# Kernel optimization log

Hardware: AMD Instinct MI355X
Metric: run time of the kernel (lower is better)

The kernel has to match this reference:

```python
import jax, jax.numpy as jnp
import numpy as np

C_IN = 256
A = 2086
H_BOARD, W_BOARD = 10, 9
S = H_BOARD * W_BOARD  # 90
E = 2                  # embed dim after 1x1 conv
NH = 2                 # num attention heads (head_dim = 1)
B = 4096
BN_EPS = 1e-5


def setup_inputs() -> dict:
    key = jax.random.key(0)
    ks = jax.random.split(key, 12)
    inp = {
        "x": jax.random.normal(ks[0], (B, C_IN, H_BOARD, W_BOARD), dtype=jnp.float32),
        # 1x1 conv, no bias: weight [out=2, in=256]
        "conv_w": jax.random.normal(ks[1], (E, C_IN), dtype=jnp.float32) * 0.05,
        # BatchNorm2d(2) params / running stats (inference-mode BN)
        "bn_gamma": jnp.ones((E,), dtype=jnp.float32),
        "bn_beta": jnp.zeros((E,), dtype=jnp.float32),
        "bn_mean": jax.random.normal(ks[2], (E,), dtype=jnp.float32) * 0.1,
        "bn_var": jax.random.uniform(ks[3], (E,), dtype=jnp.float32, minval=0.5, maxval=1.5),
        # MultiheadAttention packed in-proj: [3*E, E], bias [3*E]
        "in_proj_w": jax.random.normal(ks[4], (3 * E, E), dtype=jnp.float32) * 0.5,
        "in_proj_b": jax.random.normal(ks[5], (3 * E,), dtype=jnp.float32) * 0.05,
        "out_proj_w": jax.random.normal(ks[6], (E, E), dtype=jnp.float32) * 0.5,
        "out_proj_b": jax.random.normal(ks[7], (E,), dtype=jnp.float32) * 0.05,
        # Linear(2*90 -> 2086)
        "fc_w": jax.random.normal(ks[8], (A, E * S), dtype=jnp.float32) * 0.05,
        "fc_b": jax.random.normal(ks[9], (A,), dtype=jnp.float32) * 0.05,
    }
    return inp


def reference(x, conv_w, bn_gamma, bn_beta, bn_mean, bn_var,
              in_proj_w, in_proj_b, out_proj_w, out_proj_b, fc_w, fc_b):
    b = x.shape[0]
    # 1x1 conv (bias-free) == channel contraction: [b,256,h,w] -> [b,2,h,w]
    y = jnp.einsum('bchw,oc->bohw', x, conv_w)
    # BatchNorm2d (inference): (y - mean) / sqrt(var + eps) * gamma + beta
    scale = (bn_gamma * jax.lax.rsqrt(bn_var + BN_EPS))[None, :, None, None]
    shift = (bn_beta - bn_mean * bn_gamma * jax.lax.rsqrt(bn_var + BN_EPS))[None, :, None, None]
    y = y * scale + shift
    # [b,2,h,w] -> [b, S, 2]  (seq = board cells, feature = 2 channels)
    xf = y.reshape(b, E, S).transpose(0, 2, 1)
    # packed QKV projection
    qkv = xf @ in_proj_w.T + in_proj_b          # [b,S,3E]
    q, k, v = jnp.split(qkv, 3, axis=-1)        # each [b,S,E]
    hd = E // NH                                 # head_dim = 1
    def split_heads(t):
        return t.reshape(b, S, NH, hd).transpose(0, 2, 1, 3)  # [b,nh,S,hd]
    q, k, v = split_heads(q), split_heads(k), split_heads(v)
    scores = jnp.einsum('bhqd,bhkd->bhqk', q, k) / jnp.sqrt(jnp.float32(hd))
    attn = jax.nn.softmax(scores, axis=-1)      # [b,nh,S,S]
    o = jnp.einsum('bhqk,bhkd->bhqd', attn, v)  # [b,nh,S,hd]
    o = o.transpose(0, 2, 1, 3).reshape(b, S, E)
    o = o @ out_proj_w.T + out_proj_b           # [b,S,E]
    # [b,S,E] -> [b,E,S] -> [b, E*S], matching permute(0,2,1).view(b,-1)
    flat = o.transpose(0, 2, 1).reshape(b, E * S)
    logits = flat @ fc_w.T + fc_b               # [b, 2086]
    return logits
```

## Files before the change

kernel.cpp:

```cpp
#include <hip/hip_runtime.h>

#define C_IN    256
#define S_CELLS 90
#define A_OUT   2086
#define K_FC    180
#define K_PAD   192
#define N_PAD   2176
#define B_BATCH 4096

typedef __attribute__((ext_vector_type(8))) short short8;
typedef __attribute__((ext_vector_type(4))) float floatx4;

static __device__ __forceinline__ unsigned short f2bf(float f) {
    unsigned u = __float_as_uint(f);
    return (unsigned short)((u + 0x7FFFu + ((u >> 16) & 1u)) >> 16);
}

__global__ __launch_bounds__(384) void front_kernel(
    const float* __restrict__ x,
    const float* __restrict__ conv_w,
    const float* __restrict__ bn_gamma,
    const float* __restrict__ bn_beta,
    const float* __restrict__ bn_mean,
    const float* __restrict__ bn_var,
    const float* __restrict__ ipw,
    const float* __restrict__ ipb,
    const float* __restrict__ opw,
    const float* __restrict__ opb,
    unsigned short* __restrict__ Abf)
{
    __shared__ float4 kvpack[4][S_CELLS];

    const int sub = threadIdx.x / 96;
    const int s   = threadIdx.x % 96;
    const int b   = blockIdx.x * 4 + sub;

    float q0 = 0.f, q1 = 0.f;

    if (s < S_CELLS) {
        const float* xb = x + (size_t)b * (C_IN * S_CELLS) + s;
        float a0 = 0.f, a1 = 0.f;
        #pragma unroll 16
        for (int c = 0; c < C_IN; ++c) {
            float xv = xb[(size_t)c * S_CELLS];
            a0 = fmaf(conv_w[c], xv, a0);
            a1 = fmaf(conv_w[C_IN + c], xv, a1);
        }
        const float sc0 = bn_gamma[0] * rsqrtf(bn_var[0] + 1e-5f);
        const float sc1 = bn_gamma[1] * rsqrtf(bn_var[1] + 1e-5f);
        const float y0 = a0 * sc0 + (bn_beta[0] - bn_mean[0] * sc0);
        const float y1 = a1 * sc1 + (bn_beta[1] - bn_mean[1] * sc1);
        q0 = ipw[0] * y0 + ipw[1] * y1 + ipb[0];
        q1 = ipw[2] * y0 + ipw[3] * y1 + ipb[1];
        const float k0 = ipw[4] * y0 + ipw[5]  * y1 + ipb[2];
        const float k1 = ipw[6] * y0 + ipw[7]  * y1 + ipb[3];
        const float v0 = ipw[8] * y0 + ipw[9]  * y1 + ipb[4];
        const float v1 = ipw[10]* y0 + ipw[11] * y1 + ipb[5];
        kvpack[sub][s] = make_float4(k0, v0, k1, v1);
    }
    __syncthreads();
    if (s < S_CELLS) {
        float den0 = 0.f, num0 = 0.f, den1 = 0.f, num1 = 0.f;
        #pragma unroll 5
        for (int j = 0; j < S_CELLS; ++j) {
            const float4 kv = kvpack[sub][j];
            const float e0 = __expf(q0 * kv.x);
            const float e1 = __expf(q1 * kv.z);
            den0 += e0; num0 = fmaf(e0, kv.y, num0);
            den1 += e1; num1 = fmaf(e1, kv.w, num1);
        }
        const float o0 = num0 / den0;
        const float o1 = num1 / den1;
        const float r0 = opw[0] * o0 + opw[1] * o1 + opb[0];
        const float r1 = opw[2] * o0 + opw[3] * o1 + opb[1];
        Abf[(size_t)b * K_PAD + s]           = f2bf(r0);
        Abf[(size_t)b * K_PAD + S_CELLS + s] = f2bf(r1);
    } else {
        Abf[(size_t)b * K_PAD + 180 + (s - S_CELLS)] = 0;
        Abf[(size_t)b * K_PAD + 186 + (s - S_CELLS)] = 0;
    }
}

__global__ __launch_bounds__(192) void wconv_kernel(
    const float* __restrict__ W, unsigned short* __restrict__ Wbf)
{
    const int n = blockIdx.x;
    const int k = threadIdx.x;
    unsigned short v = 0;
    if (n < A_OUT && k < K_FC) v = f2bf(W[(size_t)n * K_FC + k]);
    Wbf[(size_t)n * K_PAD + k] = v;
}

#define BM 128
#define BN 128
#define BK 64
#define LDSROW 72

__global__ __launch_bounds__(256) void fc_mfma_kernel(
    const unsigned short* __restrict__ Abf,
    const unsigned short* __restrict__ Wbf,
    const float* __restrict__ bias,
    float* __restrict__ out)
{
    __shared__ __align__(16) unsigned short As[BM * LDSROW];
    __shared__ __align__(16) unsigned short Bs[BN * LDSROW];

    const int tid  = threadIdx.x;
    const int lane = tid & 63;
    const int wave = tid >> 6;
    const int wy   = wave >> 1;
    const int wx   = wave & 1;
    const int lrow = lane & 15;
    const int lk   = (lane >> 4) * 8;
    const int bm   = blockIdx.y * BM;
    const int bn   = blockIdx.x * BN;

    floatx4 acc[4][4] = {};

    for (int k0 = 0; k0 < K_PAD; k0 += BK) {
        for (int q = tid; q < BM * 8; q += 256) {
            const int m = q >> 3, c = q & 7;
            *(int4*)&As[m * LDSROW + c * 8] =
                *(const int4*)(Abf + (size_t)(bm + m) * K_PAD + k0 + c * 8);
            *(int4*)&Bs[m * LDSROW + c * 8] =
                *(const int4*)(Wbf + (size_t)(bn + m) * K_PAD + k0 + c * 8);
        }
        __syncthreads();

        #pragma unroll
        for (int ks = 0; ks < 2; ++ks) {
            short8 af[4], bf[4];
            #pragma unroll
            for (int t = 0; t < 4; ++t) {
                af[t] = *(const short8*)&As[(wy * 64 + t * 16 + lrow) * LDSROW + ks * 32 + lk];
                bf[t] = *(const short8*)&Bs[(wx * 64 + t * 16 + lrow) * LDSROW + ks * 32 + lk];
            }
            #pragma unroll
            for (int mt = 0; mt < 4; ++mt)
                #pragma unroll
                for (int nt = 0; nt < 4; ++nt)
                    acc[mt][nt] = __builtin_amdgcn_mfma_f32_16x16x32_bf16(
                        af[mt], bf[nt], acc[mt][nt], 0, 0, 0);
        }
        __syncthreads();
    }

    const int ccol = lane & 15;
    const int crow = (lane >> 4) * 4;
    #pragma unroll
    for (int mt = 0; mt < 4; ++mt) {
        #pragma unroll
        for (int nt = 0; nt < 4; ++nt) {
            const int n_out = bn + wx * 64 + nt * 16 + ccol;
            if (n_out >= A_OUT) continue;
            const int m_base = bm + wy * 64 + mt * 16 + crow;
            const float bv = bias[n_out];
            #pragma unroll
            for (int r = 0; r < 4; ++r)
                out[(size_t)(m_base + r) * A_OUT + n_out] = acc[mt][nt][r] + bv;
        }
    }
}

extern "C" void kernel_launch(void* const* d_in, const int* in_sizes, int n_in,
                              void* d_out, int out_size, void* d_ws, size_t ws_size,
                              hipStream_t stream) {
    const float* x        = (const float*)d_in[0];
    const float* conv_w   = (const float*)d_in[1];
    const float* bn_gamma = (const float*)d_in[2];
    const float* bn_beta  = (const float*)d_in[3];
    const float* bn_mean  = (const float*)d_in[4];
    const float* bn_var   = (const float*)d_in[5];
    const float* ipw      = (const float*)d_in[6];
    const float* ipb      = (const float*)d_in[7];
    const float* opw      = (const float*)d_in[8];
    const float* opb      = (const float*)d_in[9];
    const float* fc_w     = (const float*)d_in[10];
    const float* fc_b     = (const float*)d_in[11];
    float* out = (float*)d_out;

    unsigned short* Abf = (unsigned short*)d_ws;
    unsigned short* Wbf = (unsigned short*)((char*)d_ws + (size_t)B_BATCH * K_PAD * 2);

    front_kernel<<<dim3(B_BATCH / 4), 384, 0, stream>>>(
        x, conv_w, bn_gamma, bn_beta, bn_mean, bn_var,
        ipw, ipb, opw, opb, Abf);

    wconv_kernel<<<dim3(N_PAD), 192, 0, stream>>>(fc_w, Wbf);

    fc_mfma_kernel<<<dim3(N_PAD / BN, B_BATCH / BM), 256, 0, stream>>>(
        Abf, Wbf, fc_b, out);
}
```

Baseline: 545.2 us.

## Fuse FC weight bf16 conversion into GEMM loads and remap front kernel to one wave per board

Removes the separate weight-conversion kernel and instead converts fp32 fc_w to bf16 while staging it into LDS inside the MFMA GEMM, using zero padding for out-of-range rows and columns. This drops one launch and the round trip of the converted weights through memory. The cost is that every GEMM block redoes the conversion, 32 times per weight tile in total. The front kernel now gives each batch element one 64-lane wave that handles two cells per lane with float2 loads, and runs 8 boards per 512-thread block.

```diff
diff --git a/kernel.cpp b/kernel.cpp
--- a/kernel.cpp
+++ b/kernel.cpp
@@ -16,7 +16,7 @@
     return (unsigned short)((u + 0x7FFFu + ((u >> 16) & 1u)) >> 16);
 }
 
-__global__ __launch_bounds__(384) void front_kernel(
+__global__ __launch_bounds__(512) void front_kernel(
     const float* __restrict__ x,
     const float* __restrict__ conv_w,
     const float* __restrict__ bn_gamma,
@@ -29,66 +29,75 @@
     const float* __restrict__ opb,
     unsigned short* __restrict__ Abf)
 {
-    __shared__ float4 kvpack[4][S_CELLS];
-
-    const int sub = threadIdx.x / 96;
-    const int s   = threadIdx.x % 96;
-    const int b   = blockIdx.x * 4 + sub;
-
-    float q0 = 0.f, q1 = 0.f;
-
-    if (s < S_CELLS) {
-        const float* xb = x + (size_t)b * (C_IN * S_CELLS) + s;
-        float a0 = 0.f, a1 = 0.f;
-        #pragma unroll 16
+    __shared__ float4 kvs[8][S_CELLS];
+
+    const int wid  = threadIdx.x >> 6;
+    const int lane = threadIdx.x & 63;
+    const int b    = blockIdx.x * 8 + wid;
+
+    float qA0 = 0.f, qA1 = 0.f, qB0 = 0.f, qB1 = 0.f;
+    const int sA = 2 * lane;
+    const int sB = 2 * lane + 1;
+
+    if (lane < 45) {
+        const float2* xb2 = reinterpret_cast<const float2*>(
+                                x + (size_t)b * (C_IN * S_CELLS)) + lane;
+        float a00 = 0.f, a01 = 0.f, a10 = 0.f, a11 = 0.f;
+        #pragma unroll 8
         for (int c = 0; c < C_IN; ++c) {
-            float xv = xb[(size_t)c * S_CELLS];
-            a0 = fmaf(conv_w[c], xv, a0);
-            a1 = fmaf(conv_w[C_IN + c], xv, a1);
+            const float2 v = xb2[c * 45];
+            const float w0 = conv_w[c];
+            const float w1 = conv_w[C_IN + c];
+            a00 = fmaf(w0, v.x, a00); a01 = fmaf(w0, v.y, a01);
+            a10 = fmaf(w1, v.x, a10); a11 = fmaf(w1, v.y, a11);
         }
         const float sc0 = bn_gamma[0] * rsqrtf(bn_var[0] + 1e-5f);
         const float sc1 = bn_gamma[1] * rsqrtf(bn_var[1] + 1e-5f);
-        const float y0 = a0 * sc0 + (bn_beta[0] - bn_mean[0] * sc0);
-        const float y1 = a1 * sc1 + (bn_beta[1] - bn_mean[1] * sc1);
-        q0 = ipw[0] * y0 + ipw[1] * y1 + ipb[0];
-        q1 = ipw[2] * y0 + ipw[3] * y1 + ipb[1];
-        const float k0 = ipw[4] * y0 + ipw[5]  * y1 + ipb[2];
-        const float k1 = ipw[6] * y0 + ipw[7]  * y1 + ipb[3];
-        const float v0 = ipw[8] * y0 + ipw[9]  * y1 + ipb[4];
-        const float v1 = ipw[10]* y0 + ipw[11] * y1 + ipb[5];
-        kvpack[sub][s] = make_float4(k0, v0, k1, v1);
+        const float sh0 = bn_beta[0] - bn_mean[0] * sc0;
+        const float sh1 = bn_beta[1] - bn_mean[1] * sc1;
+        const float yA0 = a00 * sc0 + sh0, yA1 = a10 * sc1 + sh1;
+        const float yB0 = a01 * sc0 + sh0, yB1 = a11 * sc1 + sh1;
+
+        qA0 = ipw[0] * yA0 + ipw[1] * yA1 + ipb[0];
+        qA1 = ipw[2] * yA0 + ipw[3] * yA1 + ipb[1];
+        qB0 = ipw[0] * yB0 + ipw[1] * yB1 + ipb[0];
+        qB1 = ipw[2] * yB0 + ipw[3] * yB1 + ipb[1];
+
+        kvs[wid][sA] = make_float4(
+            ipw[4] * yA0 + ipw[5]  * yA1 + ipb[2],
+            ipw[8] * yA0 + ipw[9]  * yA1 + ipb[4],
+            ipw[6] * yA0 + ipw[7]  * yA1 + ipb[3],
+            ipw[10]* yA0 + ipw[11] * yA1 + ipb[5]);
+        kvs[wid][sB] = make_float4(
+            ipw[4] * yB0 + ipw[5]  * yB1 + ipb[2],
+            ipw[8] * yB0 + ipw[9]  * yB1 + ipb[4],
+            ipw[6] * yB0 + ipw[7]  * yB1 + ipb[3],
+            ipw[10]* yB0 + ipw[11] * yB1 + ipb[5]);
     }
     __syncthreads();
-    if (s < S_CELLS) {
-        float den0 = 0.f, num0 = 0.f, den1 = 0.f, num1 = 0.f;
+
+    if (lane < 45) {
+        float dA0 = 0.f, nA0 = 0.f, dA1 = 0.f, nA1 = 0.f;
+        float dB0 = 0.f, nB0 = 0.f, dB1 = 0.f, nB1 = 0.f;
         #pragma unroll 5
         for (int j = 0; j < S_CELLS; ++j) {
-            const float4 kv = kvpack[sub][j];
-            const float e0 = __expf(q0 * kv.x);
-            const float e1 = __expf(q1 * kv.z);
-            den0 += e0; num0 = fmaf(e0, kv.y, num0);
-            den1 += e1; num1 = fmaf(e1, kv.w, num1);
-        }
-        const float o0 = num0 / den0;
-        const float o1 = num1 / den1;
-        const float r0 = opw[0] * o0 + opw[1] * o1 + opb[0];
-        const float r1 = opw[2] * o0 + opw[3] * o1 + opb[1];
-        Abf[(size_t)b * K_PAD + s]           = f2bf(r0);
-        Abf[(size_t)b * K_PAD + S_CELLS + s] = f2bf(r1);
-    } else {
-        Abf[(size_t)b * K_PAD + 180 + (s - S_CELLS)] = 0;
-        Abf[(size_t)b * K_PAD + 186 + (s - S_CELLS)] = 0;
-    }
-}
-
-__global__ __launch_bounds__(192) void wconv_kernel(
-    const float* __restrict__ W, unsigned short* __restrict__ Wbf)
-{
-    const int n = blockIdx.x;
-    const int k = threadIdx.x;
-    unsigned short v = 0;
-    if (n < A_OUT && k < K_FC) v = f2bf(W[(size_t)n * K_FC + k]);
-    Wbf[(size_t)n * K_PAD + k] = v;
+            const float4 kv = kvs[wid][j];
+            float e;
+            e = __expf(qA0 * kv.x); dA0 += e; nA0 = fmaf(e, kv.y, nA0);
+            e = __expf(qA1 * kv.z); dA1 += e; nA1 = fmaf(e, kv.w, nA1);
+            e = __expf(qB0 * kv.x); dB0 += e; nB0 = fmaf(e, kv.y, nB0);
+            e = __expf(qB1 * kv.z); dB1 += e; nB1 = fmaf(e, kv.w, nB1);
+        }
+        const float oA0 = nA0 / dA0, oA1 = nA1 / dA1;
+        const float oB0 = nB0 / dB0, oB1 = nB1 / dB1;
+        unsigned short* ab = Abf + (size_t)b * K_PAD;
+        ab[sA]           = f2bf(opw[0] * oA0 + opw[1] * oA1 + opb[0]);
+        ab[S_CELLS + sA] = f2bf(opw[2] * oA0 + opw[3] * oA1 + opb[1]);
+        ab[sB]           = f2bf(opw[0] * oB0 + opw[1] * oB1 + opb[0]);
+        ab[S_CELLS + sB] = f2bf(opw[2] * oB0 + opw[3] * oB1 + opb[1]);
+    } else if (lane < 57) {
+        Abf[(size_t)b * K_PAD + 135 + lane] = 0;
+    }
 }
 
 #define BM 128
@@ -98,7 +107,7 @@
 
 __global__ __launch_bounds__(256) void fc_mfma_kernel(
     const unsigned short* __restrict__ Abf,
-    const unsigned short* __restrict__ Wbf,
+    const float* __restrict__ W,
     const float* __restrict__ bias,
     float* __restrict__ out)
 {
@@ -122,8 +131,24 @@
             const int m = q >> 3, c = q & 7;
             *(int4*)&As[m * LDSROW + c * 8] =
                 *(const int4*)(Abf + (size_t)(bm + m) * K_PAD + k0 + c * 8);
-            *(int4*)&Bs[m * LDSROW + c * 8] =
-                *(const int4*)(Wbf + (size_t)(bn + m) * K_PAD + k0 + c * 8);
+
+            const int n  = bn + m;
+            const int kb = k0 + c * 8;
+            unsigned short h[8];
+            if (n < A_OUT && kb + 7 < K_FC) {
+                const float4 f0 = *(const float4*)(W + (size_t)n * K_FC + kb);
+                const float4 f1 = *(const float4*)(W + (size_t)n * K_FC + kb + 4);
+                h[0] = f2bf(f0.x); h[1] = f2bf(f0.y); h[2] = f2bf(f0.z); h[3] = f2bf(f0.w);
+                h[4] = f2bf(f1.x); h[5] = f2bf(f1.y); h[6] = f2bf(f1.z); h[7] = f2bf(f1.w);
+            } else {
+                #pragma unroll
+                for (int t = 0; t < 8; ++t) {
+                    const int k = kb + t;
+                    h[t] = (n < A_OUT && k < K_FC)
+                           ? f2bf(W[(size_t)n * K_FC + k]) : (unsigned short)0;
+                }
+            }
+            *(int4*)&Bs[m * LDSROW + c * 8] = *(const int4*)h;
         }
         __syncthreads();
 
@@ -180,14 +205,11 @@
     float* out = (float*)d_out;
 
     unsigned short* Abf = (unsigned short*)d_ws;
-    unsigned short* Wbf = (unsigned short*)((char*)d_ws + (size_t)B_BATCH * K_PAD * 2);
-
-    front_kernel<<<dim3(B_BATCH / 4), 384, 0, stream>>>(
+
+    front_kernel<<<dim3(B_BATCH / 8), 512, 0, stream>>>(
         x, conv_w, bn_gamma, bn_beta, bn_mean, bn_var,
         ipw, ipb, opw, opb, Abf);
 
-    wconv_kernel<<<dim3(N_PAD), 192, 0, stream>>>(fc_w, Wbf);
-
     fc_mfma_kernel<<<dim3(N_PAD / BN, B_BATCH / BM), 256, 0, stream>>>(
-        Abf, Wbf, fc_b, out);
-}
+        Abf, fc_w, fc_b, out);
+}
```

After: 552.1 us. Within noise of the previous version (+1.3%).
